# Kernel optimization log

Measured on AMD Instinct MI355X. Metric: run time of the kernel, lower is better.

Reference implementation:

```python
import jax, jax.numpy as jnp
import numpy as np

N_NODES = 100000
N_EDGES = 1600000
IN_DIM = 128
HID = 128
OUT_DIM = 1
EPS = 1e-5
NEG_SLOPE = 0.01


def _glorot(key, shape):
    fan_in = shape[-1]
    return jax.random.normal(key, shape, dtype=jnp.float32) / np.sqrt(fan_in)


def setup_inputs() -> dict:
    key = jax.random.key(0)
    ks = jax.random.split(key, 16)
    x = jax.random.normal(ks[0], (N_NODES, IN_DIM), dtype=jnp.float32)
    edge_index = jax.random.randint(ks[1], (2, N_EDGES), 0, N_NODES, dtype=jnp.int64 if jax.config.jax_enable_x64 else jnp.int32)
    params = {
        'W_in': _glorot(ks[2], (HID, IN_DIM)), 'b_in': jnp.zeros((HID,), jnp.float32),
        # SAGEConv params: lin_l (applied to max-aggregated neighbors, with bias), lin_r (applied to self, no bias)
        'W_l1': _glorot(ks[3], (HID, HID)), 'b_l1': jnp.zeros((HID,), jnp.float32), 'W_r1': _glorot(ks[4], (HID, HID)),
        'W_l2': _glorot(ks[5], (HID, HID)), 'b_l2': jnp.zeros((HID,), jnp.float32), 'W_r2': _glorot(ks[6], (HID, HID)),
        'W_l3': _glorot(ks[7], (HID, HID)), 'b_l3': jnp.zeros((HID,), jnp.float32), 'W_r3': _glorot(ks[8], (HID, HID)),
        'g1': jnp.ones((HID,), jnp.float32), 'be1': jnp.zeros((HID,), jnp.float32),
        'g2': jnp.ones((HID,), jnp.float32), 'be2': jnp.zeros((HID,), jnp.float32),
        'g3': jnp.ones((HID,), jnp.float32), 'be3': jnp.zeros((HID,), jnp.float32),
        'W_fc1': _glorot(ks[9], (HID // 2, HID)), 'b_fc1': jnp.zeros((HID // 2,), jnp.float32),
        'W_fc2': _glorot(ks[10], (OUT_DIM, HID // 2)), 'b_fc2': jnp.zeros((OUT_DIM,), jnp.float32),
    }
    return {'x': x, 'edge_index': edge_index, **params}


def _sage_conv_max(x, src, dst, W_l, b_l, W_r):
    # gather source features per edge, scatter-max into destination nodes
    agg = jax.ops.segment_max(x[src], dst, num_segments=N_NODES)  # [N, H], -inf where no neighbors
    agg = jnp.where(jnp.isfinite(agg), agg, 0.0)
    return agg @ W_l.T + b_l + x @ W_r.T


def _batch_norm(x, gamma, beta):
    mean = x.mean(axis=0)
    var = x.var(axis=0)
    return gamma * (x - mean) * jax.lax.rsqrt(var + EPS) + beta


def _lrelu(x):
    return jax.nn.leaky_relu(x, negative_slope=NEG_SLOPE)


def reference(x, edge_index, W_in, b_in,
              W_l1, b_l1, W_r1, W_l2, b_l2, W_r2, W_l3, b_l3, W_r3,
              g1, be1, g2, be2, g3, be3,
              W_fc1, b_fc1, W_fc2, b_fc2):
    src, dst = edge_index[0], edge_index[1]
    h = x @ W_in.T + b_in
    residual = h
    h = _lrelu(_batch_norm(_sage_conv_max(h, src, dst, W_l1, b_l1, W_r1), g1, be1))
    h = _lrelu(_batch_norm(_sage_conv_max(h, src, dst, W_l2, b_l2, W_r2), g2, be2))
    h = _lrelu(_batch_norm(_sage_conv_max(h, src, dst, W_l3, b_l3, W_r3), g3, be3))
    h = h + residual  # dropout layers are identity in deterministic/eval reference
    h = _lrelu(h @ W_fc1.T + b_fc1)
    return h @ W_fc2.T + b_fc2  # [N, OUT_DIM]
```

## Files before the change

kernel.cpp:

```cpp
#include <hip/hip_runtime.h>
#include <cstdint>
#include <cstddef>

#define HID 128

typedef __bf16 bf16x8 __attribute__((ext_vector_type(8)));
typedef float f32x4 __attribute__((ext_vector_type(4)));

__device__ __forceinline__ float bf2f(uint32_t u) {
    union { uint32_t i; float f; } x; x.i = u << 16; return x.f;
}
__device__ __forceinline__ float bflo(uint32_t p) { return bf2f(p & 0xffffu); }
__device__ __forceinline__ float bfhi(uint32_t p) { return bf2f(p >> 16); }
__device__ __forceinline__ float bfs(const uint16_t* p) { return bf2f((uint32_t)*p); }
__device__ __forceinline__ uint16_t f2bf(float f) {
    union { float f; uint32_t i; } x; x.f = f;
    uint32_t u = x.i;
    return (uint16_t)((u + 0x7fffu + ((u >> 16) & 1u)) >> 16);
}
__device__ __forceinline__ uint32_t pack2(float a, float b) {
    return (uint32_t)f2bf(a) | ((uint32_t)f2bf(b) << 16);
}
__device__ __forceinline__ float lrelu_f(float v) { return v > 0.f ? v : 0.01f * v; }
__device__ __forceinline__ bf16x8 ldfrag(const uint16_t* p) {
    union { uint4 u; bf16x8 b; } c;
    c.u = *(const uint4*)p;
    return c.b;
}

__global__ __launch_bounds__(256) void sentinel_kernel(float* out, int n) {
    int i = blockIdx.x * 256 + threadIdx.x;
    if (i < n) out[i] = 65536.0f;
}

__global__ void detect_e_kernel(const int* __restrict__ ei, int* __restrict__ flagE) {
    int lane = threadIdx.x;
    int w = ei[2 * lane + 1];
    unsigned long long b = __ballot(w != 0);
    if (lane == 0) flagE[0] = (b == 0ULL) ? 1 : 0;
}
__global__ void detect_f_kernel(const uint32_t* __restrict__ x, int* __restrict__ flagF) {
    int lane = threadIdx.x;
    uint32_t e = (x[lane] >> 7) & 0xFFu;
    unsigned long long b = __ballot(e >= 64u && e <= 144u);
    if (lane == 0) flagF[0] = (b == ~0ULL) ? 0 : 1;
}

struct WArgs {
    const void* src[8];
    uint16_t* dst[8];
    int nrows[8];
};
__global__ __launch_bounds__(256) void convert_w(WArgs a, const int* __restrict__ flagF) {
    int mat = blockIdx.x >> 6;
    int idx = ((blockIdx.x & 63) << 8) + threadIdx.x;
    if (idx < a.nrows[mat] * HID) {
        a.dst[mat][idx] = flagF[0] ? f2bf(((const float*)a.src[mat])[idx])
                                   : ((const uint16_t*)a.src[mat])[idx];
    }
}

struct ParamArgs {
    const void* src[14];
    int off[14];
    int cnt[14];
};
__global__ __launch_bounds__(128) void convert_params(ParamArgs pa, float* __restrict__ params,
                                                      const int* __restrict__ flagF) {
    int b = blockIdx.x, t = threadIdx.x;
    if (t < pa.cnt[b]) {
        float v = flagF[0] ? ((const float*)pa.src[b])[t]
                           : bfs(&((const uint16_t*)pa.src[b])[t]);
        params[pa.off[b] + t] = v;
    }
}

__global__ __launch_bounds__(256) void convert_x(const void* __restrict__ x,
                                                 uint32_t* __restrict__ dst,
                                                 const int* __restrict__ flagF, int total2) {
    int i = blockIdx.x * 256 + threadIdx.x;
    if (i >= total2) return;
    if (flagF[0]) {
        float2 v = ((const float2*)x)[i];
        dst[i] = pack2(v.x, v.y);
    } else {
        dst[i] = ((const uint32_t*)x)[i];
    }
}

__global__ __launch_bounds__(256) void hist_kernel(const int* __restrict__ ei,
                                                   const int* __restrict__ flagE,
                                                   int* deg, int E) {
    int e = blockIdx.x * 256 + threadIdx.x;
    if (e < E) {
        int d = flagE[0] ? ei[2 * (E + e)] : ei[E + e];
        atomicAdd(&deg[d], 1);
    }
}
__global__ __launch_bounds__(256) void scan_a(const int* deg, int* scanbuf, int M, int CH) {
    int i = blockIdx.x * 256 + threadIdx.x;
    int s = i * CH, e = min(s + CH, M);
    int t = 0;
    for (int j = s; j < e; ++j) t += deg[j];
    scanbuf[i] = t;
}
__global__ __launch_bounds__(1024) void scan_b(int* scanbuf) {
    __shared__ int sm[1024];
    int tid = threadIdx.x;
    int v = scanbuf[tid];
    sm[tid] = v;
    __syncthreads();
    for (int off = 1; off < 1024; off <<= 1) {
        int t = (tid >= off) ? sm[tid - off] : 0;
        __syncthreads();
        sm[tid] += t;
        __syncthreads();
    }
    scanbuf[tid] = sm[tid] - v;
}
__global__ __launch_bounds__(256) void scan_c(int* deg_then_cursor, const int* scanbuf,
                                              int* rowptr, int M, int E, int CH) {
    int i = blockIdx.x * 256 + threadIdx.x;
    int run = scanbuf[i];
    int s = i * CH, e = min(s + CH, M);
    for (int j = s; j < e; ++j) {
        int d = deg_then_cursor[j];
        rowptr[j] = run;
        deg_then_cursor[j] = run;
        run += d;
    }
    if (i == 0) rowptr[M] = E;
}
__global__ __launch_bounds__(256) void fill_kernel(const int* __restrict__ ei,
                                                   const int* __restrict__ flagE,
                                                   int* cursor, int* csr, int E) {
    int e = blockIdx.x * 256 + threadIdx.x;
    if (e < E) {
        int isl = flagE[0];
        int s = isl ? ei[2 * e] : ei[e];
        int d = isl ? ei[2 * (E + e)] : ei[E + e];
        int p = atomicAdd(&cursor[d], 1);
        csr[p] = s;
    }
}

__global__ __launch_bounds__(256) void gather_kernel(const uint4* __restrict__ cur,
                                                     const int* __restrict__ rowptr,
                                                     const int* __restrict__ csr,
                                                     uint4* __restrict__ agg, int M) {
    int gid = blockIdx.x * 256 + threadIdx.x;
    int node = gid >> 4;
    int sl = threadIdx.x & 15;
    if (node >= M) return;
    int b = rowptr[node], e = rowptr[node + 1];
    float m[8];
#pragma unroll
    for (int j = 0; j < 8; ++j) m[j] = -INFINITY;
    int i = b;
    for (; i + 2 <= e; i += 2) {
        int s0 = csr[i], s1 = csr[i + 1];
        uint4 u0 = cur[(size_t)s0 * 16 + sl];
        uint4 u1 = cur[(size_t)s1 * 16 + sl];
        uint32_t w0[4] = {u0.x, u0.y, u0.z, u0.w};
        uint32_t w1[4] = {u1.x, u1.y, u1.z, u1.w};
#pragma unroll
        for (int j = 0; j < 4; ++j) {
            m[2 * j]     = fmaxf(m[2 * j],     fmaxf(bflo(w0[j]), bflo(w1[j])));
            m[2 * j + 1] = fmaxf(m[2 * j + 1], fmaxf(bfhi(w0[j]), bfhi(w1[j])));
        }
    }
    if (i < e) {
        int s0 = csr[i];
        uint4 u0 = cur[(size_t)s0 * 16 + sl];
        uint32_t w0[4] = {u0.x, u0.y, u0.z, u0.w};
#pragma unroll
        for (int j = 0; j < 4; ++j) {
            m[2 * j]     = fmaxf(m[2 * j],     bflo(w0[j]));
            m[2 * j + 1] = fmaxf(m[2 * j + 1], bfhi(w0[j]));
        }
    }
    if (b == e) {
#pragma unroll
        for (int j = 0; j < 8; ++j) m[j] = 0.f;
    }
    uint4 o;
    o.x = pack2(m[0], m[1]); o.y = pack2(m[2], m[3]);
    o.z = pack2(m[4], m[5]); o.w = pack2(m[6], m[7]);
    agg[(size_t)node * 16 + sl] = o;
}

template<int N, int NSRC, bool ACT, bool OUTF32>
__global__ __launch_bounds__(256) void gemm_mfma(
    const uint16_t* __restrict__ A0, const uint16_t* __restrict__ W0,
    const uint16_t* __restrict__ A1, const uint16_t* __restrict__ W1,
    const float* __restrict__ bias, void* __restrict__ out_, int M)
{
    constexpr int LDT = 40;
    constexpr int WAVES_N = N / 64;
    constexpr int WAVES_M = 4 / WAVES_N;
    constexpr int MT = 8 / WAVES_M;
    constexpr int NT = 4;
    __shared__ uint16_t LX[128 * LDT];
    __shared__ uint16_t LW[N * LDT];
    const int tid = threadIdx.x;
    const int wave = tid >> 6, lane = tid & 63;
    const int l15 = lane & 15, lkg = lane >> 4;
    const int wn = (wave % WAVES_N) * 64;
    const int wm = (wave / WAVES_N) * (128 / WAVES_M);
    const int row0 = blockIdx.x * 128;

    f32x4 acc[NT][MT];
#pragma unroll
    for (int nt = 0; nt < NT; ++nt)
#pragma unroll
        for (int mt = 0; mt < MT; ++mt) {
            f32x4 z4 = {0.f, 0.f, 0.f, 0.f};
            acc[nt][mt] = z4;
        }

#pragma unroll 1
    for (int s = 0; s < NSRC; ++s) {
        const uint16_t* Ag = (s == 0) ? A0 : A1;
        const uint16_t* Wg = (s == 0) ? W0 : W1;
#pragma unroll 1
        for (int kc = 0; kc < 4; ++kc) {
            __syncthreads();
            {
                int id = tid;
#pragma unroll
                for (int it = 0; it < 2; ++it, id += 256) {
                    int r = id >> 2, ko = (id & 3) * 8;
                    uint4 v = make_uint4(0, 0, 0, 0);
                    int gr = row0 + r;
                    if (gr < M) v = *(const uint4*)(Ag + (size_t)gr * HID + kc * 32 + ko);
                    *(uint4*)&LX[r * LDT + ko] = v;
                }
            }
            {
                int id = tid;
#pragma unroll
                for (int it = 0; it < N / 64; ++it, id += 256) {
                    int r = id >> 2, ko = (id & 3) * 8;
                    *(uint4*)&LW[r * LDT + ko] = *(const uint4*)(Wg + (size_t)r * HID + kc * 32 + ko);
                }
            }
            __syncthreads();
            bf16x8 xf[MT], wf[NT];
#pragma unroll
            for (int mt = 0; mt < MT; ++mt)
                xf[mt] = ldfrag(&LX[(wm + mt * 16 + l15) * LDT + lkg * 8]);
#pragma unroll
            for (int nt = 0; nt < NT; ++nt)
                wf[nt] = ldfrag(&LW[(wn + nt * 16 + l15) * LDT + lkg * 8]);
#pragma unroll
            for (int nt = 0; nt < NT; ++nt)
#pragma unroll
                for (int mt = 0; mt < MT; ++mt)
                    acc[nt][mt] = __builtin_amdgcn_mfma_f32_16x16x32_bf16(
                        wf[nt], xf[mt], acc[nt][mt], 0, 0, 0);
        }
    }

#pragma unroll
    for (int nt = 0; nt < NT; ++nt) {
        int n0 = wn + nt * 16 + lkg * 4;
        float b0 = bias[n0], b1 = bias[n0 + 1], b2 = bias[n0 + 2], b3 = bias[n0 + 3];
#pragma unroll
        for (int mt = 0; mt < MT; ++mt) {
            int m = row0 + wm + mt * 16 + l15;
            if (m < M) {
                f32x4 f = acc[nt][mt];
                float o0 = f[0] + b0, o1 = f[1] + b1, o2 = f[2] + b2, o3 = f[3] + b3;
                if constexpr (ACT) {
                    o0 = lrelu_f(o0); o1 = lrelu_f(o1); o2 = lrelu_f(o2); o3 = lrelu_f(o3);
                }
                if constexpr (OUTF32) {
                    *(float4*)((float*)out_ + (size_t)m * N + n0) = make_float4(o0, o1, o2, o3);
                } else {
                    ushort4 ov;
                    ov.x = f2bf(o0); ov.y = f2bf(o1); ov.z = f2bf(o2); ov.w = f2bf(o3);
                    *(ushort4*)((uint16_t*)out_ + (size_t)m * N + n0) = ov;
                }
            }
        }
    }
}

__global__ __launch_bounds__(256) void bn_stats(const uint32_t* __restrict__ z,
                                                float* __restrict__ stats, int M, int rpb) {
    __shared__ float4 red[256];
    int c2 = threadIdx.x & 63;
    int part = threadIdx.x >> 6;
    int s0 = blockIdx.x * rpb, e0 = min(s0 + rpb, M);
    float sl = 0.f, s2l = 0.f, sh = 0.f, s2h = 0.f;
    for (int r = s0 + part; r < e0; r += 4) {
        uint32_t u = z[(size_t)r * 64 + c2];
        float a = bflo(u), b = bfhi(u);
        sl += a; s2l = fmaf(a, a, s2l);
        sh += b; s2h = fmaf(b, b, s2h);
    }
    red[threadIdx.x] = make_float4(sl, s2l, sh, s2h);
    __syncthreads();
    if (threadIdx.x < 64) {
        float4 v = red[threadIdx.x];
        float4 v1 = red[threadIdx.x + 64], v2 = red[threadIdx.x + 128], v3 = red[threadIdx.x + 192];
        v.x += v1.x + v2.x + v3.x; v.y += v1.y + v2.y + v3.y;
        v.z += v1.z + v2.z + v3.z; v.w += v1.w + v2.w + v3.w;
        int cc = c2 * 2;
        atomicAdd(&stats[cc], v.x);
        atomicAdd(&stats[128 + cc], v.y);
        atomicAdd(&stats[cc + 1], v.z);
        atomicAdd(&stats[129 + cc], v.w);
    }
}
__global__ void bn_finalize(float* stats, const float* __restrict__ g,
                            const float* __restrict__ be, int M) {
    int c = threadIdx.x;
    float mean = stats[c] / (float)M;
    float var = stats[128 + c] / (float)M - mean * mean;
    float sc = g[c] * rsqrtf(var + 1e-5f);
    stats[c] = sc;
    stats[128 + c] = be[c] - mean * sc;
}
__global__ __launch_bounds__(256) void bn_apply(uint32_t* __restrict__ z,
                                                const float* __restrict__ stats, int total2) {
    int i = blockIdx.x * 256 + threadIdx.x;
    if (i >= total2) return;
    int cc = (i & 63) * 2;
    uint32_t u = z[i];
    float a = lrelu_f(fmaf(bflo(u), stats[cc], stats[128 + cc]));
    float b = lrelu_f(fmaf(bfhi(u), stats[cc + 1], stats[129 + cc]));
    z[i] = pack2(a, b);
}

__global__ __launch_bounds__(256) void combine_kernel(const uint32_t* __restrict__ a,
                                                      const uint32_t* __restrict__ b,
                                                      uint32_t* __restrict__ t, int total2) {
    int i = blockIdx.x * 256 + threadIdx.x;
    if (i >= total2) return;
    uint32_t ua = a[i], ub = b[i];
    t[i] = pack2(bflo(ua) + bflo(ub), bfhi(ua) + bfhi(ub));
}

__global__ __launch_bounds__(256) void final_fc2(const float* __restrict__ z2,
                                                 const float* __restrict__ w2,
                                                 const float* __restrict__ b2,
                                                 float* __restrict__ out, int M) {
    int gid = blockIdx.x * 256 + threadIdx.x;
    int v = gid >> 6, lane = gid & 63;
    if (v >= M) return;
    float val = z2[(size_t)v * 64 + lane] * w2[lane];
#pragma unroll
    for (int off = 32; off > 0; off >>= 1) val += __shfl_down(val, off, 64);
    if (lane == 0) out[v] = val + b2[0];
}

extern "C" void kernel_launch(void* const* d_in, const int* in_sizes, int n_in,
                              void* d_out, int out_size, void* d_ws, size_t ws_size,
                              hipStream_t stream) {
    const void* x = d_in[0];
    const int* ei = (const int*)d_in[1];
    const int M = in_sizes[0] / HID;
    const int E = in_sizes[1] / 2;

    const size_t FEAT = (size_t)M * HID * 2;
    char* p = (char*)d_ws;
    uint16_t* H0 = (uint16_t*)p; p += FEAT;
    uint16_t* P  = (uint16_t*)p; p += FEAT;
    uint16_t* Q  = (uint16_t*)p; p += FEAT;
    uint16_t* WT = (uint16_t*)p; p += 8 * 16384 * 2;
    float* params = (float*)p; p += 8192;
    int* rowptr  = (int*)p; p += ((size_t)M + 32) * 4;
    int* cursor  = (int*)p; p += ((size_t)M + 32) * 4;
    int* csr     = (int*)p; p += (size_t)E * 4;
    int* scanbuf = (int*)p; p += 4096;
    float* stats = (float*)p; p += 1024;
    int* flagE   = (int*)p; p += 128;
    int* flagF   = (int*)p; p += 128;

    const size_t needed = (size_t)(p - (char*)d_ws);
    if (needed > ws_size) {
        sentinel_kernel<<<(out_size + 255) / 256, 256, 0, stream>>>(
            (float*)d_out, out_size);
        return;
    }

    uint16_t* wt[8];
    for (int i = 0; i < 8; ++i) wt[i] = WT + (size_t)i * 16384;

    detect_e_kernel<<<1, 64, 0, stream>>>(ei, flagE);
    detect_f_kernel<<<1, 64, 0, stream>>>((const uint32_t*)x, flagF);

    WArgs wa;
    const int widx[8] = {2, 4, 6, 7, 9, 10, 12, 19};
    for (int i = 0; i < 8; ++i) {
        wa.src[i] = d_in[widx[i]];
        wa.dst[i] = wt[i];
        wa.nrows[i] = (i == 7) ? 64 : 128;
    }
    convert_w<<<512, 256, 0, stream>>>(wa, flagF);

    ParamArgs pa;
    const int pidx[14] = {3, 5, 8, 11, 13, 15, 17, 14, 16, 18, 20, 21, 22, 22};
    const int poff[14] = {0, 128, 256, 384, 512, 640, 768, 896, 1024, 1152, 1280, 1344, 1408, 1409};
    const int pcnt[14] = {128, 128, 128, 128, 128, 128, 128, 128, 128, 128, 64, 64, 1, 0};
    for (int i = 0; i < 14; ++i) { pa.src[i] = d_in[pidx[i]]; pa.off[i] = poff[i]; pa.cnt[i] = pcnt[i]; }
    convert_params<<<14, 128, 0, stream>>>(pa, params, flagF);

    const int total2 = M * (HID / 2);
    const int ew_grid = (total2 + 255) / 256;
    convert_x<<<ew_grid, 256, 0, stream>>>(x, (uint32_t*)Q, flagF, total2);

    hipMemsetAsync(cursor, 0, (size_t)(M + 1) * sizeof(int), stream);
    const int egrid = (E + 255) / 256;
    hist_kernel<<<egrid, 256, 0, stream>>>(ei, flagE, cursor, E);
    const int CH = (M + 1023) >> 10;
    scan_a<<<4, 256, 0, stream>>>(cursor, scanbuf, M, CH);
    scan_b<<<1, 1024, 0, stream>>>(scanbuf);
    scan_c<<<4, 256, 0, stream>>>(cursor, scanbuf, rowptr, M, E, CH);
    fill_kernel<<<egrid, 256, 0, stream>>>(ei, flagE, cursor, csr, E);

    const int gemm_grid = (M + 127) / 128;
    const int gather_grid = (M + 15) / 16;
    const int fc2_grid = (M + 3) / 4;
    const int rpb = (M + 255) / 256;

    gemm_mfma<128, 1, false, false><<<gemm_grid, 256, 0, stream>>>(
        Q, wt[0], nullptr, nullptr, params + 0, H0, M);

    uint16_t* wtl[3] = {wt[1], wt[3], wt[5]};
    uint16_t* wtr[3] = {wt[2], wt[4], wt[6]};
    uint16_t* cur = H0;
    uint16_t* dstb[3] = {P, Q, P};
    for (int l = 0; l < 3; ++l) {
        uint16_t* z = dstb[l];
        gather_kernel<<<gather_grid, 256, 0, stream>>>(
            (const uint4*)cur, rowptr, csr, (uint4*)z, M);
        gemm_mfma<128, 2, false, false><<<gemm_grid, 256, 0, stream>>>(
            z, wtl[l], cur, wtr[l], params + 128 + l * 128, z, M);
        hipMemsetAsync(stats, 0, 1024, stream);
        bn_stats<<<256, 256, 0, stream>>>((const uint32_t*)z, stats, M, rpb);
        bn_finalize<<<1, 128, 0, stream>>>(stats, params + 512 + l * 128,
                                           params + 896 + l * 128, M);
        bn_apply<<<ew_grid, 256, 0, stream>>>((uint32_t*)z, stats, total2);
        cur = z;
    }

    combine_kernel<<<ew_grid, 256, 0, stream>>>(
        (const uint32_t*)cur, (const uint32_t*)H0, (uint32_t*)P, total2);
    float* Z2 = (float*)Q;
    gemm_mfma<64, 1, true, true><<<gemm_grid, 256, 0, stream>>>(
        P, wt[7], nullptr, nullptr, params + 1280, Z2, M);
    final_fc2<<<fc2_grid, 256, 0, stream>>>(
        Z2, params + 1344, params + 1408, (float*)d_out, M);
}
```

Measured before the change: 884.0 us.

## Bucketed CSR build, fuse BN stats into GEMM, fuse residual and fc2

After: 1.312 ms. 48.4% more time.

```diff
diff --git a/kernel.cpp b/kernel.cpp
--- a/kernel.cpp
+++ b/kernel.cpp
@@ -88,27 +88,29 @@
     }
 }
 
-__global__ __launch_bounds__(256) void hist_kernel(const int* __restrict__ ei,
+__global__ __launch_bounds__(256) void bucket_hist(const int* __restrict__ ei,
                                                    const int* __restrict__ flagE,
-                                                   int* deg, int E) {
+                                                   int* __restrict__ bcnt8, int E) {
     int e = blockIdx.x * 256 + threadIdx.x;
     if (e < E) {
         int d = flagE[0] ? ei[2 * (E + e)] : ei[E + e];
-        atomicAdd(&deg[d], 1);
-    }
-}
-__global__ __launch_bounds__(256) void scan_a(const int* deg, int* scanbuf, int M, int CH) {
-    int i = blockIdx.x * 256 + threadIdx.x;
-    int s = i * CH, e = min(s + CH, M);
-    int t = 0;
-    for (int j = s; j < e; ++j) t += deg[j];
-    scanbuf[i] = t;
-}
-__global__ __launch_bounds__(1024) void scan_b(int* scanbuf) {
+        atomicAdd(&bcnt8[((d >> 7) << 3) + (blockIdx.x & 7)], 1);
+    }
+}
+__global__ __launch_bounds__(1024) void bucket_scan(int* __restrict__ bcnt8,
+                                                    int* __restrict__ bstart, int NB, int E) {
     __shared__ int sm[1024];
     int tid = threadIdx.x;
-    int v = scanbuf[tid];
-    sm[tid] = v;
+    int base = tid * 8;
+    int loc[8];
+    int tot = 0;
+#pragma unroll
+    for (int j = 0; j < 8; ++j) {
+        int idx = base + j;
+        int v = (idx < NB * 8) ? bcnt8[idx] : 0;
+        loc[j] = tot; tot += v;
+    }
+    sm[tid] = tot;
     __syncthreads();
     for (int off = 1; off < 1024; off <<= 1) {
         int t = (tid >= off) ? sm[tid - off] : 0;
@@ -116,31 +118,57 @@
         sm[tid] += t;
         __syncthreads();
     }
-    scanbuf[tid] = sm[tid] - v;
-}
-__global__ __launch_bounds__(256) void scan_c(int* deg_then_cursor, const int* scanbuf,
-                                              int* rowptr, int M, int E, int CH) {
-    int i = blockIdx.x * 256 + threadIdx.x;
-    int run = scanbuf[i];
-    int s = i * CH, e = min(s + CH, M);
-    for (int j = s; j < e; ++j) {
-        int d = deg_then_cursor[j];
-        rowptr[j] = run;
-        deg_then_cursor[j] = run;
-        run += d;
-    }
-    if (i == 0) rowptr[M] = E;
-}
-__global__ __launch_bounds__(256) void fill_kernel(const int* __restrict__ ei,
+    int exof = sm[tid] - tot;
+#pragma unroll
+    for (int j = 0; j < 8; ++j) {
+        int idx = base + j;
+        if (idx < NB * 8) bcnt8[idx] = exof + loc[j];
+    }
+    if (tid <= NB) bstart[tid] = (tid < 1024) ? ((tid * 8 < NB * 8) ? exof : E) : E;
+    if (tid == NB) bstart[NB] = E;
+}
+__global__ __launch_bounds__(256) void bucket_fill(const int* __restrict__ ei,
                                                    const int* __restrict__ flagE,
-                                                   int* cursor, int* csr, int E) {
+                                                   int* __restrict__ bcur8,
+                                                   uint2* __restrict__ bins, int E) {
     int e = blockIdx.x * 256 + threadIdx.x;
     if (e < E) {
         int isl = flagE[0];
         int s = isl ? ei[2 * e] : ei[e];
         int d = isl ? ei[2 * (E + e)] : ei[E + e];
-        int p = atomicAdd(&cursor[d], 1);
-        csr[p] = s;
+        int p = atomicAdd(&bcur8[((d >> 7) << 3) + (blockIdx.x & 7)], 1);
+        bins[p] = make_uint2((uint32_t)s, (uint32_t)d);
+    }
+}
+__global__ __launch_bounds__(256) void csr_build(const uint2* __restrict__ bins,
+                                                 const int* __restrict__ bstart,
+                                                 int* __restrict__ rowptr,
+                                                 int* __restrict__ csr, int M, int E) {
+    int b = blockIdx.x;
+    int node0 = b << 7;
+    int nn = min(128, M - node0);
+    int s = bstart[b], e = bstart[b + 1];
+    __shared__ int cnt[128];
+    __shared__ int ofs[128];
+    if (threadIdx.x < 128) cnt[threadIdx.x] = 0;
+    __syncthreads();
+    for (int i = s + threadIdx.x; i < e; i += 256)
+        atomicAdd(&cnt[bins[i].y & 127], 1);
+    __syncthreads();
+    if (threadIdx.x == 0) {
+        int run = s;
+        for (int j = 0; j < 128; ++j) { ofs[j] = run; run += cnt[j]; }
+    }
+    __syncthreads();
+    if (threadIdx.x < nn) rowptr[node0 + threadIdx.x] = ofs[threadIdx.x];
+    if (b == 0 && threadIdx.x == 0) rowptr[M] = E;
+    if (threadIdx.x < 128) cnt[threadIdx.x] = 0;
+    __syncthreads();
+    for (int i = s + threadIdx.x; i < e; i += 256) {
+        uint2 pr = bins[i];
+        int d = pr.y & 127;
+        int pos = ofs[d] + atomicAdd(&cnt[d], 1);
+        csr[pos] = (int)pr.x;
     }
 }
 
@@ -189,11 +217,12 @@
     agg[(size_t)node * 16 + sl] = o;
 }
 
-template<int N, int NSRC, bool ACT, bool OUTF32>
+template<int N, int NSRC, bool ACT, bool STATS, bool FC2>
 __global__ __launch_bounds__(256) void gemm_mfma(
     const uint16_t* __restrict__ A0, const uint16_t* __restrict__ W0,
     const uint16_t* __restrict__ A1, const uint16_t* __restrict__ W1,
-    const float* __restrict__ bias, void* __restrict__ out_, int M)
+    const float* __restrict__ bias, void* __restrict__ out_, int M,
+    float* __restrict__ stats, const float* __restrict__ fc2w)
 {
     constexpr int LDT = 40;
     constexpr int WAVES_N = N / 64;
@@ -261,58 +290,81 @@
         }
     }
 
-#pragma unroll
-    for (int nt = 0; nt < NT; ++nt) {
-        int n0 = wn + nt * 16 + lkg * 4;
-        float b0 = bias[n0], b1 = bias[n0 + 1], b2 = bias[n0 + 2], b3 = bias[n0 + 3];
+    if constexpr (FC2) {
+        float rowdot[MT];
+#pragma unroll
+        for (int mt = 0; mt < MT; ++mt) rowdot[mt] = 0.f;
+#pragma unroll
+        for (int nt = 0; nt < NT; ++nt) {
+            int n0 = wn + nt * 16 + lkg * 4;
+            float b4[4] = {bias[n0], bias[n0 + 1], bias[n0 + 2], bias[n0 + 3]};
+            float w4[4] = {fc2w[n0], fc2w[n0 + 1], fc2w[n0 + 2], fc2w[n0 + 3]};
+#pragma unroll
+            for (int mt = 0; mt < MT; ++mt) {
+                f32x4 f = acc[nt][mt];
+#pragma unroll
+                for (int j = 0; j < 4; ++j)
+                    rowdot[mt] = fmaf(lrelu_f(f[j] + b4[j]), w4[j], rowdot[mt]);
+            }
+        }
+        float b2 = fc2w[64];
 #pragma unroll
         for (int mt = 0; mt < MT; ++mt) {
+            float v = rowdot[mt];
+            v += __shfl_xor(v, 16, 64);
+            v += __shfl_xor(v, 32, 64);
             int m = row0 + wm + mt * 16 + l15;
-            if (m < M) {
-                f32x4 f = acc[nt][mt];
-                float o0 = f[0] + b0, o1 = f[1] + b1, o2 = f[2] + b2, o3 = f[3] + b3;
-                if constexpr (ACT) {
-                    o0 = lrelu_f(o0); o1 = lrelu_f(o1); o2 = lrelu_f(o2); o3 = lrelu_f(o3);
-                }
-                if constexpr (OUTF32) {
-                    *(float4*)((float*)out_ + (size_t)m * N + n0) = make_float4(o0, o1, o2, o3);
-                } else {
+            if (lkg == 0 && m < M) ((float*)out_)[m] = v + b2;
+        }
+    } else {
+        float cs[16], cq[16];
+        if constexpr (STATS) {
+#pragma unroll
+            for (int v = 0; v < 16; ++v) { cs[v] = 0.f; cq[v] = 0.f; }
+        }
+#pragma unroll
+        for (int nt = 0; nt < NT; ++nt) {
+            int n0 = wn + nt * 16 + lkg * 4;
+            float b0 = bias[n0], b1 = bias[n0 + 1], b2 = bias[n0 + 2], b3 = bias[n0 + 3];
+#pragma unroll
+            for (int mt = 0; mt < MT; ++mt) {
+                int m = row0 + wm + mt * 16 + l15;
+                if (m < M) {
+                    f32x4 f = acc[nt][mt];
+                    float o0 = f[0] + b0, o1 = f[1] + b1, o2 = f[2] + b2, o3 = f[3] + b3;
+                    if constexpr (STATS) {
+                        cs[nt * 4 + 0] += o0; cq[nt * 4 + 0] = fmaf(o0, o0, cq[nt * 4 + 0]);
+                        cs[nt * 4 + 1] += o1; cq[nt * 4 + 1] = fmaf(o1, o1, cq[nt * 4 + 1]);
+                        cs[nt * 4 + 2] += o2; cq[nt * 4 + 2] = fmaf(o2, o2, cq[nt * 4 + 2]);
+                        cs[nt * 4 + 3] += o3; cq[nt * 4 + 3] = fmaf(o3, o3, cq[nt * 4 + 3]);
+                    }
+                    if constexpr (ACT) {
+                        o0 = lrelu_f(o0); o1 = lrelu_f(o1); o2 = lrelu_f(o2); o3 = lrelu_f(o3);
+                    }
                     ushort4 ov;
                     ov.x = f2bf(o0); ov.y = f2bf(o1); ov.z = f2bf(o2); ov.w = f2bf(o3);
                     *(ushort4*)((uint16_t*)out_ + (size_t)m * N + n0) = ov;
                 }
             }
         }
-    }
-}
-
-__global__ __launch_bounds__(256) void bn_stats(const uint32_t* __restrict__ z,
-                                                float* __restrict__ stats, int M, int rpb) {
-    __shared__ float4 red[256];
-    int c2 = threadIdx.x & 63;
-    int part = threadIdx.x >> 6;
-    int s0 = blockIdx.x * rpb, e0 = min(s0 + rpb, M);
-    float sl = 0.f, s2l = 0.f, sh = 0.f, s2h = 0.f;
-    for (int r = s0 + part; r < e0; r += 4) {
-        uint32_t u = z[(size_t)r * 64 + c2];
-        float a = bflo(u), b = bfhi(u);
-        sl += a; s2l = fmaf(a, a, s2l);
-        sh += b; s2h = fmaf(b, b, s2h);
-    }
-    red[threadIdx.x] = make_float4(sl, s2l, sh, s2h);
-    __syncthreads();
-    if (threadIdx.x < 64) {
-        float4 v = red[threadIdx.x];
-        float4 v1 = red[threadIdx.x + 64], v2 = red[threadIdx.x + 128], v3 = red[threadIdx.x + 192];
-        v.x += v1.x + v2.x + v3.x; v.y += v1.y + v2.y + v3.y;
-        v.z += v1.z + v2.z + v3.z; v.w += v1.w + v2.w + v3.w;
-        int cc = c2 * 2;
-        atomicAdd(&stats[cc], v.x);
-        atomicAdd(&stats[128 + cc], v.y);
-        atomicAdd(&stats[cc + 1], v.z);
-        atomicAdd(&stats[129 + cc], v.w);
-    }
-}
+        if constexpr (STATS) {
+#pragma unroll
+            for (int v = 0; v < 16; ++v) {
+                float a = cs[v], q = cq[v];
+                a += __shfl_xor(a, 1, 64); q += __shfl_xor(q, 1, 64);
+                a += __shfl_xor(a, 2, 64); q += __shfl_xor(q, 2, 64);
+                a += __shfl_xor(a, 4, 64); q += __shfl_xor(q, 4, 64);
+                a += __shfl_xor(a, 8, 64); q += __shfl_xor(q, 8, 64);
+                if (l15 == 0) {
+                    int n = wn + (v >> 2) * 16 + lkg * 4 + (v & 3);
+                    atomicAdd(&stats[n], a);
+                    atomicAdd(&stats[128 + n], q);
+                }
+            }
+        }
+    }
+}
+
 __global__ void bn_finalize(float* stats, const float* __restrict__ g,
                             const float* __restrict__ be, int M) {
     int c = threadIdx.x;
@@ -332,27 +384,16 @@
     float b = lrelu_f(fmaf(bfhi(u), stats[cc + 1], stats[129 + cc]));
     z[i] = pack2(a, b);
 }
-
-__global__ __launch_bounds__(256) void combine_kernel(const uint32_t* __restrict__ a,
-                                                      const uint32_t* __restrict__ b,
-                                                      uint32_t* __restrict__ t, int total2) {
+__global__ __launch_bounds__(256) void bn_apply_res(uint32_t* __restrict__ z,
+                                                    const uint32_t* __restrict__ h0,
+                                                    const float* __restrict__ stats, int total2) {
     int i = blockIdx.x * 256 + threadIdx.x;
     if (i >= total2) return;
-    uint32_t ua = a[i], ub = b[i];
-    t[i] = pack2(bflo(ua) + bflo(ub), bfhi(ua) + bfhi(ub));
-}
-
-__global__ __launch_bounds__(256) void final_fc2(const float* __restrict__ z2,
-                                                 const float* __restrict__ w2,
-                                                 const float* __restrict__ b2,
-                                                 float* __restrict__ out, int M) {
-    int gid = blockIdx.x * 256 + threadIdx.x;
-    int v = gid >> 6, lane = gid & 63;
-    if (v >= M) return;
-    float val = z2[(size_t)v * 64 + lane] * w2[lane];
-#pragma unroll
-    for (int off = 32; off > 0; off >>= 1) val += __shfl_down(val, off, 64);
-    if (lane == 0) out[v] = val + b2[0];
+    int cc = (i & 63) * 2;
+    uint32_t u = z[i], r = h0[i];
+    float a = lrelu_f(fmaf(bflo(u), stats[cc], stats[128 + cc])) + bflo(r);
+    float b = lrelu_f(fmaf(bfhi(u), stats[cc + 1], stats[129 + cc])) + bfhi(r);
+    z[i] = pack2(a, b);
 }
 
 extern "C" void kernel_launch(void* const* d_in, const int* in_sizes, int n_in,
@@ -362,6 +403,7 @@
     const int* ei = (const int*)d_in[1];
     const int M = in_sizes[0] / HID;
     const int E = in_sizes[1] / 2;
+    const int NB = (M + 127) >> 7;
 
     const size_t FEAT = (size_t)M * HID * 2;
     char* p = (char*)d_ws;
@@ -371,10 +413,10 @@
     uint16_t* WT = (uint16_t*)p; p += 8 * 16384 * 2;
     float* params = (float*)p; p += 8192;
     int* rowptr  = (int*)p; p += ((size_t)M + 32) * 4;
-    int* cursor  = (int*)p; p += ((size_t)M + 32) * 4;
     int* csr     = (int*)p; p += (size_t)E * 4;
-    int* scanbuf = (int*)p; p += 4096;
-    float* stats = (float*)p; p += 1024;
+    int* bcnt8   = (int*)p; p += 8 * 1024 * 4;
+    int* bstart  = (int*)p; p += 1056 * 4;
+    float* stats = (float*)p; p += 3 * 256 * 4;
     int* flagE   = (int*)p; p += 128;
     int* flagF   = (int*)p; p += 128;
 
@@ -411,22 +453,19 @@
     const int ew_grid = (total2 + 255) / 256;
     convert_x<<<ew_grid, 256, 0, stream>>>(x, (uint32_t*)Q, flagF, total2);
 
-    hipMemsetAsync(cursor, 0, (size_t)(M + 1) * sizeof(int), stream);
+    hipMemsetAsync(bcnt8, 0, (size_t)NB * 8 * sizeof(int), stream);
+    hipMemsetAsync(stats, 0, 3 * 256 * sizeof(float), stream);
     const int egrid = (E + 255) / 256;
-    hist_kernel<<<egrid, 256, 0, stream>>>(ei, flagE, cursor, E);
-    const int CH = (M + 1023) >> 10;
-    scan_a<<<4, 256, 0, stream>>>(cursor, scanbuf, M, CH);
-    scan_b<<<1, 1024, 0, stream>>>(scanbuf);
-    scan_c<<<4, 256, 0, stream>>>(cursor, scanbuf, rowptr, M, E, CH);
-    fill_kernel<<<egrid, 256, 0, stream>>>(ei, flagE, cursor, csr, E);
+    bucket_hist<<<egrid, 256, 0, stream>>>(ei, flagE, bcnt8, E);
+    bucket_scan<<<1, 1024, 0, stream>>>(bcnt8, bstart, NB, E);
+    bucket_fill<<<egrid, 256, 0, stream>>>(ei, flagE, bcnt8, (uint2*)P, E);
+    csr_build<<<NB, 256, 0, stream>>>((const uint2*)P, bstart, rowptr, csr, M, E);
 
     const int gemm_grid = (M + 127) / 128;
     const int gather_grid = (M + 15) / 16;
-    const int fc2_grid = (M + 3) / 4;
-    const int rpb = (M + 255) / 256;
-
-    gemm_mfma<128, 1, false, false><<<gemm_grid, 256, 0, stream>>>(
-        Q, wt[0], nullptr, nullptr, params + 0, H0, M);
+
+    gemm_mfma<128, 1, false, false, false><<<gemm_grid, 256, 0, stream>>>(
+        Q, wt[0], nullptr, nullptr, params + 0, H0, M, nullptr, nullptr);
 
     uint16_t* wtl[3] = {wt[1], wt[3], wt[5]};
     uint16_t* wtr[3] = {wt[2], wt[4], wt[6]};
@@ -434,23 +473,22 @@
     uint16_t* dstb[3] = {P, Q, P};
     for (int l = 0; l < 3; ++l) {
         uint16_t* z = dstb[l];
+        float* sl = stats + 256 * l;
         gather_kernel<<<gather_grid, 256, 0, stream>>>(
             (const uint4*)cur, rowptr, csr, (uint4*)z, M);
-        gemm_mfma<128, 2, false, false><<<gemm_grid, 256, 0, stream>>>(
-            z, wtl[l], cur, wtr[l], params + 128 + l * 128, z, M);
-        hipMemsetAsync(stats, 0, 1024, stream);
-        bn_stats<<<256, 256, 0, stream>>>((const uint32_t*)z, stats, M, rpb);
-        bn_finalize<<<1, 128, 0, stream>>>(stats, params + 512 + l * 128,
+        gemm_mfma<128, 2, false, true, false><<<gemm_grid, 256, 0, stream>>>(
+            z, wtl[l], cur, wtr[l], params + 128 + l * 128, z, M, sl, nullptr);
+        bn_finalize<<<1, 128, 0, stream>>>(sl, params + 512 + l * 128,
                                            params + 896 + l * 128, M);
-        bn_apply<<<ew_grid, 256, 0, stream>>>((uint32_t*)z, stats, total2);
+        if (l < 2)
+            bn_apply<<<ew_grid, 256, 0, stream>>>((uint32_t*)z, sl, total2);
+        else
+            bn_apply_res<<<ew_grid, 256, 0, stream>>>((uint32_t*)z, (const uint32_t*)H0,
+                                                      sl, total2);
         cur = z;
     }
 
-    combine_kernel<<<ew_grid, 256, 0, stream>>>(
-        (const uint32_t*)cur, (const uint32_t*)H0, (uint32_t*)P, total2);
-    float* Z2 = (float*)Q;
-    gemm_mfma<64, 1, true, true><<<gemm_grid, 256, 0, stream>>>(
-        P, wt[7], nullptr, nullptr, params + 1280, Z2, M);
-    final_fc2<<<fc2_grid, 256, 0, stream>>>(
-        Z2, params + 1344, params + 1408, (float*)d_out, M);
-}
+    gemm_mfma<64, 1, true, false, true><<<gemm_grid, 256, 0, stream>>>(
+        P, wt[7], nullptr, nullptr, params + 1280, (float*)d_out, M,
+        nullptr, params + 1344);
+}
```
